# Kernel tuning notes

Hardware: AMD Instinct MI355X
Metric: run time of the kernel (lower is better)

The kernel has to match this reference:

```python
import jax, jax.numpy as jnp
import numpy as np

BITS = 4
GROUP_SIZE = 128
IN_FEATURES = 4096
OUT_FEATURES = 11008
PACKED_DIM = IN_FEATURES * BITS // 32  # 512
NUM_GROUPS = IN_FEATURES // GROUP_SIZE  # 32


def setup_inputs() -> dict:
    key = jax.random.key(0)
    k1, k2, k3, k4, k5 = jax.random.split(key, 5)
    x = jax.random.normal(k1, (4, 2048, IN_FEATURES), dtype=jnp.float32)
    # packed uint32 words stored as int32 bit pattern (full 32-bit entropy)
    weight_packed = jax.random.randint(
        k2, (OUT_FEATURES, PACKED_DIM), jnp.iinfo(jnp.int32).min, jnp.iinfo(jnp.int32).max, dtype=jnp.int32
    )
    scales = jax.random.uniform(k3, (OUT_FEATURES, NUM_GROUPS), dtype=jnp.float32, minval=0.01, maxval=0.1)
    biases = jax.random.normal(k4, (OUT_FEATURES, NUM_GROUPS), dtype=jnp.float32) * 0.1
    bias = jax.random.normal(k5, (OUT_FEATURES,), dtype=jnp.float32) * 0.1
    return {"x": x, "weight_packed": weight_packed, "scales": scales, "biases": biases, "bias": bias}


def _unpack_int4(weight_packed):
    # (O, packed_dim) int32 -> view as uint32, extract 8 nibbles per word -> (O, infeatures)
    w = weight_packed.astype(jnp.uint32)
    shifts = (jnp.arange(32 // BITS, dtype=jnp.uint32) * BITS)  # [0,4,...,28]
    mask = jnp.uint32((1 << BITS) - 1)
    nibbles = (w[:, :, None] >> shifts[None, None, :]) & mask  # (O, packed, 8)
    return nibbles.reshape(w.shape[0], -1)[:, :IN_FEATURES]


def _dequant_weight(weight_packed, scales, biases):
    intw = _unpack_int4(weight_packed).astype(jnp.float32)  # (O, I)
    s = jnp.repeat(scales, GROUP_SIZE, axis=1)[:, :IN_FEATURES]  # (O, I)
    b = jnp.repeat(biases, GROUP_SIZE, axis=1)[:, :IN_FEATURES]
    return s * intw + b


def reference(x, weight_packed, scales, biases, bias):
    W = _dequant_weight(weight_packed, scales, biases)  # (O, I)
    out = jnp.einsum("bsi,oi->bso", x, W)
    return out + bias
```

## Files before the change

### kernel.cpp

```cpp
#include <hip/hip_runtime.h>

#define K_DIM 4096
#define N_DIM 11008
#define M_DIM 8192
#define K2B (K_DIM * 2)

#define BM 128
#define BN 128
#define BK 32

typedef __bf16 bf16x8_t __attribute__((ext_vector_type(8)));
typedef float f32x4_t __attribute__((ext_vector_type(4)));

#define GLD_LDS16(g, l)                                                        \
  __builtin_amdgcn_global_load_lds(                                            \
      (const __attribute__((address_space(1))) void*)(g),                      \
      (__attribute__((address_space(3))) void*)(l), 16, 0, 0)

__global__ void dequant_w(const int* __restrict__ wp, const float* __restrict__ sc,
                          const float* __restrict__ bg, __bf16* __restrict__ W) {
  const int tid = blockIdx.x * 256 + threadIdx.x;
  const unsigned w = (unsigned)wp[tid];
  const int row = tid >> 9;
  const int word = tid & 511;
  const int g = word >> 4;
  const float s = sc[row * 32 + g];
  const float b = bg[row * 32 + g];
  bf16x8_t v;
#pragma unroll
  for (int i = 0; i < 8; ++i)
    v[i] = (__bf16)(s * (float)((w >> (4 * i)) & 15u) + b);
  ((bf16x8_t*)W)[tid] = v;
}

__global__ void cvt_x(const float* __restrict__ X, __bf16* __restrict__ Xb) {
  const size_t t = (size_t)blockIdx.x * 256 + threadIdx.x;
  const float4* s = ((const float4*)X) + 2 * t;
  const float4 f0 = s[0], f1 = s[1];
  bf16x8_t v;
  v[0] = (__bf16)f0.x; v[1] = (__bf16)f0.y; v[2] = (__bf16)f0.z; v[3] = (__bf16)f0.w;
  v[4] = (__bf16)f1.x; v[5] = (__bf16)f1.y; v[6] = (__bf16)f1.z; v[7] = (__bf16)f1.w;
  ((bf16x8_t*)Xb)[t] = v;
}

__device__ __forceinline__ void stage2(const char* g, char* l) {
  GLD_LDS16(g, l);
  GLD_LDS16(g + (size_t)64 * K2B, l + 8192);
}

template <int AM, int AN>
__device__ __forceinline__ void mfma_quad(f32x4_t (&acc)[8][4],
                                          const bf16x8_t (&A)[4][2],
                                          const bf16x8_t (&B)[2][2]) {
#pragma unroll
  for (int mi = 0; mi < 4; ++mi)
#pragma unroll
    for (int nj = 0; nj < 2; ++nj)
#pragma unroll
      for (int ks = 0; ks < 2; ++ks)
        acc[AM + mi][AN + nj] = __builtin_amdgcn_mfma_f32_16x16x32_bf16(
            A[mi][ks], B[nj][ks], acc[AM + mi][AN + nj], 0, 0, 0);
}

__device__ __forceinline__ void rd_a(bf16x8_t (&d)[4][2], const char* p, int s0, int s1) {
#pragma unroll
  for (int mi = 0; mi < 4; ++mi) {
    d[mi][0] = *(const bf16x8_t*)(p + mi * 2048 + s0);
    d[mi][1] = *(const bf16x8_t*)(p + mi * 2048 + s1);
  }
}
__device__ __forceinline__ void rd_b(bf16x8_t (&d)[2][2], const char* p, int s0, int s1) {
#pragma unroll
  for (int nj = 0; nj < 2; ++nj) {
    d[nj][0] = *(const bf16x8_t*)(p + nj * 2048 + s0);
    d[nj][1] = *(const bf16x8_t*)(p + nj * 2048 + s1);
  }
}

#define PH_SYNC_IN()                                                           \
  do {                                                                         \
    __builtin_amdgcn_s_barrier();                                              \
    asm volatile("s_waitcnt lgkmcnt(0)" ::: "memory");                         \
    __builtin_amdgcn_sched_barrier(0);                                         \
    __builtin_amdgcn_s_setprio(1);                                             \
  } while (0)
#define PH_SYNC_OUT()                                                          \
  do {                                                                         \
    __builtin_amdgcn_s_setprio(0);                                             \
    __builtin_amdgcn_sched_barrier(0);                                         \
    __builtin_amdgcn_s_barrier();                                              \
  } while (0)

__launch_bounds__(512, 2)
__global__ void qgemm8(const __bf16* __restrict__ Ab, const __bf16* __restrict__ Bw,
                       const float* __restrict__ bias, float* __restrict__ C) {
  __shared__ alignas(128) char smem[131072];
  const int tid = threadIdx.x;
  const int lane = tid & 63;
  const int wave = tid >> 6;
  const int wm = wave >> 2;
  const int wn = wave & 3;
  const int l16 = lane & 15;
  const int quad = lane >> 4;

  int bid = (int)blockIdx.x;
  bid = (bid & 7) * 172 + (bid >> 3);
  const int m0 = (bid / 43) * 256;
  const int n0 = (bid % 43) * 256;

  const int rr = tid >> 3;
  const int sw = ((tid & 7) ^ (rr & 7)) * 16;
  const char* gA = (const char*)Ab + (size_t)(m0 + rr) * K2B + sw;
  const char* gB = (const char*)Bw + (size_t)(n0 + rr) * K2B + sw;
  char* lA = smem + wave * 1024;
  char* lB = smem + 32768 + wave * 1024;

  const int s0 = ((0 + quad) ^ (l16 & 7)) * 16;
  const int s1 = ((4 + quad) ^ (l16 & 7)) * 16;
  const char* fA = smem + (wm * 64 + l16) * 128;
  const char* fB = smem + 32768 + (wn * 32 + l16) * 128;

  f32x4_t acc[8][4];
#pragma unroll
  for (int i = 0; i < 8; ++i)
#pragma unroll
    for (int j = 0; j < 4; ++j) acc[i][j] = (f32x4_t){0.f, 0.f, 0.f, 0.f};

  stage2(gA, lA);
  stage2(gA + (size_t)128 * K2B, lA + 16384);
  stage2(gB, lB);
  stage2(gB + (size_t)128 * K2B, lB + 16384);
  stage2(gA + 128, lA + 65536);
  stage2(gA + (size_t)128 * K2B + 128, lA + 65536 + 16384);
  stage2(gB + 128, lB + 65536);
  asm volatile("s_waitcnt vmcnt(6)" ::: "memory");
  __builtin_amdgcn_s_barrier();

  bf16x8_t fa0[4][2], fa1[4][2], fb0[2][2], fb1[2][2];

#pragma unroll 1
  for (int it = 0; it < 32; ++it) {
    const size_t o1 = (size_t)(2 * it + 1) * 128;
    const int tt2 = 2 * it + 2, tt3 = 2 * it + 3;
    const size_t o2 = (size_t)(tt2 < 64 ? tt2 : 63) * 128;
    const size_t o3 = (size_t)(tt3 < 64 ? tt3 : 63) * 128;

    rd_a(fa0, fA, s0, s1);
    rd_b(fb0, fB, s0, s1);
    stage2(gB + (size_t)128 * K2B + o1, lB + 65536 + 16384);
    PH_SYNC_IN();
    mfma_quad<0, 0>(acc, fa0, fb0);
    PH_SYNC_OUT();

    rd_a(fa1, fA + 16384, s0, s1);
    stage2(gA + o2, lA);
    PH_SYNC_IN();
    mfma_quad<4, 0>(acc, fa1, fb0);
    PH_SYNC_OUT();

    rd_b(fb1, fB + 16384, s0, s1);
    stage2(gA + (size_t)128 * K2B + o2, lA + 16384);
    PH_SYNC_IN();
    mfma_quad<4, 2>(acc, fa1, fb1);
    PH_SYNC_OUT();

    stage2(gB + o2, lB);
    asm volatile("s_waitcnt vmcnt(6)" ::: "memory");
    __builtin_amdgcn_s_barrier();
    __builtin_amdgcn_sched_barrier(0);
    __builtin_amdgcn_s_setprio(1);
    mfma_quad<0, 2>(acc, fa0, fb1);
    PH_SYNC_OUT();

    rd_a(fa0, fA + 65536, s0, s1);
    rd_b(fb0, fB + 65536, s0, s1);
    stage2(gB + (size_t)128 * K2B + o2, lB + 16384);
    PH_SYNC_IN();
    mfma_quad<0, 0>(acc, fa0, fb0);
    PH_SYNC_OUT();

    rd_a(fa1, fA + 65536 + 16384, s0, s1);
    stage2(gA + o3, lA + 65536);
    PH_SYNC_IN();
    mfma_quad<4, 0>(acc, fa1, fb0);
    PH_SYNC_OUT();

    rd_b(fb1, fB + 65536 + 16384, s0, s1);
    stage2(gA + (size_t)128 * K2B + o3, lA + 65536 + 16384);
    PH_SYNC_IN();
    mfma_quad<4, 2>(acc, fa1, fb1);
    PH_SYNC_OUT();

    stage2(gB + o3, lB + 65536);
    asm volatile("s_waitcnt vmcnt(6)" ::: "memory");
    __builtin_amdgcn_s_barrier();
    __builtin_amdgcn_sched_barrier(0);
    __builtin_amdgcn_s_setprio(1);
    mfma_quad<0, 2>(acc, fa0, fb1);
    PH_SYNC_OUT();
  }

  asm volatile("s_waitcnt vmcnt(0)" ::: "memory");

#pragma unroll
  for (int an = 0; an < 4; ++an) {
    const int n = n0 + (an >> 1) * 128 + wn * 32 + (an & 1) * 16 + l16;
    const float bv = bias[n];
#pragma unroll
    for (int am = 0; am < 8; ++am) {
      const int m = m0 + (am >> 2) * 128 + wm * 64 + (am & 3) * 16 + quad * 4;
#pragma unroll
      for (int r = 0; r < 4; ++r)
        C[(size_t)(m + r) * N_DIM + n] = acc[am][an][r] + bv;
    }
  }
}

template <int AMODE>
__launch_bounds__(256)
__global__ void qgemm(const __bf16* __restrict__ Ab, const float* __restrict__ Af,
                      const __bf16* __restrict__ Bw, const float* __restrict__ bias,
                      float* __restrict__ C) {
  __shared__ __bf16 As[BM * BK];
  __shared__ __bf16 Bs[BN * BK];

  const int tid = threadIdx.x;
  const int wave = tid >> 6;
  const int lane = tid & 63;
  const int l16 = lane & 15;
  const int quad = lane >> 4;
  const int wm = wave >> 1;
  const int wn = wave & 1;
  const int n0 = blockIdx.x * BN;
  const int m0 = blockIdx.y * BM;

  f32x4_t acc[4][4];
#pragma unroll
  for (int i = 0; i < 4; ++i)
#pragma unroll
    for (int j = 0; j < 4; ++j) acc[i][j] = (f32x4_t){0.f, 0.f, 0.f, 0.f};

  const int skq = lane & 3;
  const __bf16* gB0 =
      Bw + (size_t)(n0 + wave * 32 + (lane >> 2)) * K_DIM + skq * 8;
  __bf16* lB0 = Bs + (wave * 32) * BK;

  const __bf16* gA0 =
      (AMODE == 0) ? Ab + (size_t)(m0 + wave * 32 + (lane >> 2)) * K_DIM + skq * 8
                   : nullptr;
  __bf16* lA0 = As + (wave * 32) * BK;

  const int ar = tid >> 2;
  const int akq = tid & 3;
  const float* gX0 =
      (AMODE == 1) ? Af + (size_t)(m0 + ar) * K_DIM + akq * 8 : nullptr;
  __bf16* lAf = As + ar * BK + akq * 8;

  for (int kt = 0; kt < K_DIM; kt += BK) {
    __syncthreads();
    GLD_LDS16(gB0 + kt, lB0);
    GLD_LDS16(gB0 + kt + (size_t)16 * K_DIM, lB0 + 16 * BK);
    if (AMODE == 0) {
      GLD_LDS16(gA0 + kt, lA0);
      GLD_LDS16(gA0 + kt + (size_t)16 * K_DIM, lA0 + 16 * BK);
    } else {
#pragma unroll
      for (int p = 0; p < 2; ++p) {
        const float4* s = (const float4*)(gX0 + (size_t)p * 64 * K_DIM + kt);
        const float4 f0 = s[0], f1 = s[1];
        bf16x8_t v;
        v[0] = (__bf16)f0.x; v[1] = (__bf16)f0.y;
        v[2] = (__bf16)f0.z; v[3] = (__bf16)f0.w;
        v[4] = (__bf16)f1.x; v[5] = (__bf16)f1.y;
        v[6] = (__bf16)f1.z; v[7] = (__bf16)f1.w;
        *(bf16x8_t*)(lAf + p * 64 * BK) = v;
      }
    }
    __syncthreads();

    bf16x8_t fa[4], fb[4];
#pragma unroll
    for (int t = 0; t < 4; ++t)
      fa[t] = *(const bf16x8_t*)(As + (wm * 64 + t * 16 + l16) * BK + quad * 8);
#pragma unroll
    for (int t = 0; t < 4; ++t)
      fb[t] = *(const bf16x8_t*)(Bs + (wn * 64 + t * 16 + l16) * BK + quad * 8);
#pragma unroll
    for (int i = 0; i < 4; ++i)
#pragma unroll
      for (int j = 0; j < 4; ++j)
        acc[i][j] =
            __builtin_amdgcn_mfma_f32_16x16x32_bf16(fa[i], fb[j], acc[i][j], 0, 0, 0);
  }

#pragma unroll
  for (int j = 0; j < 4; ++j) {
    const int n = n0 + wn * 64 + j * 16 + l16;
    const float bv = bias[n];
#pragma unroll
    for (int i = 0; i < 4; ++i) {
      const int mb = m0 + wm * 64 + i * 16 + quad * 4;
#pragma unroll
      for (int r = 0; r < 4; ++r)
        C[(size_t)(mb + r) * N_DIM + n] = acc[i][j][r] + bv;
    }
  }
}

__global__ void qgemm_naive(const float* __restrict__ X, const int* __restrict__ WP,
                            const float* __restrict__ S, const float* __restrict__ BG,
                            const float* __restrict__ bias, float* __restrict__ C) {
  const int n = blockIdx.x * 256 + threadIdx.x;
  const int m = blockIdx.y;
  const float* x = X + (size_t)m * K_DIM;
  float acc = 0.f;
  for (int g = 0; g < 32; ++g) {
    const float s = S[n * 32 + g];
    const float b = BG[n * 32 + g];
    for (int wd = 0; wd < 16; ++wd) {
      const unsigned w = (unsigned)WP[n * 512 + g * 16 + wd];
      const int kb = g * 128 + wd * 8;
#pragma unroll
      for (int i = 0; i < 8; ++i)
        acc += (s * (float)((w >> (4 * i)) & 15u) + b) * x[kb + i];
    }
  }
  C[(size_t)m * N_DIM + n] = acc + bias[n];
}

extern "C" void kernel_launch(void* const* d_in, const int* in_sizes, int n_in,
                              void* d_out, int out_size, void* d_ws, size_t ws_size,
                              hipStream_t stream) {
  const float* X = (const float*)d_in[0];
  const int* WP = (const int*)d_in[1];
  const float* S = (const float*)d_in[2];
  const float* BG = (const float*)d_in[3];
  const float* BIAS = (const float*)d_in[4];
  float* C = (float*)d_out;

  const size_t needW = (size_t)N_DIM * K_DIM * 2;
  const size_t needX = (size_t)M_DIM * K_DIM * 2;

  if (ws_size >= needW + needX) {
    __bf16* W = (__bf16*)d_ws;
    __bf16* Xb = (__bf16*)((char*)d_ws + needW);
    dequant_w<<<(N_DIM * 512) / 256, 256, 0, stream>>>(WP, S, BG, W);
    cvt_x<<<(M_DIM * K_DIM) / (256 * 8), 256, 0, stream>>>(X, Xb);
    qgemm8<<<dim3((N_DIM / 256) * (M_DIM / 256)), 512, 0, stream>>>(Xb, W, BIAS, C);
  } else if (ws_size >= needW) {
    __bf16* W = (__bf16*)d_ws;
    dequant_w<<<(N_DIM * 512) / 256, 256, 0, stream>>>(WP, S, BG, W);
    qgemm<1><<<dim3(N_DIM / BN, M_DIM / BM), 256, 0, stream>>>(nullptr, X, W, BIAS, C);
  } else {
    qgemm_naive<<<dim3(N_DIM / 256, M_DIM), 256, 0, stream>>>(X, WP, S, BG, BIAS, C);
  }
}
```

Baseline: 1.065 ms.

## Split-K the tail GEMM tiles with atomic accumulation to balance the last wave

The 96 output tiles that would otherwise form a partial last wave are each split into two half-K blocks. The first 1280 tiles run at full K depth as before. A new init kernel first writes the bias into the tail region of C, and each half-K block then atomically adds its partial accumulators into that region. The aim is to cut wave-quantization idle time at the end of the GEMM. The cost is an extra kernel launch, float atomics on the tail tiles, and run-to-run nondeterministic summation order there.

```diff
diff --git a/kernel.cpp b/kernel.cpp
--- a/kernel.cpp
+++ b/kernel.cpp
@@ -41,6 +41,15 @@
   v[0] = (__bf16)f0.x; v[1] = (__bf16)f0.y; v[2] = (__bf16)f0.z; v[3] = (__bf16)f0.w;
   v[4] = (__bf16)f1.x; v[5] = (__bf16)f1.y; v[6] = (__bf16)f1.z; v[7] = (__bf16)f1.w;
   ((bf16x8_t*)Xb)[t] = v;
+}
+
+__global__ void init_ctail(const float* __restrict__ bias, float* __restrict__ C) {
+  const int t = 1280 + (blockIdx.x >> 8);
+  const int mi = blockIdx.x & 255;
+  const int m0 = (t / 43) * 256;
+  const int n0 = (t % 43) * 256;
+  const int n = n0 + threadIdx.x;
+  C[(size_t)(m0 + mi) * N_DIM + n] = bias[n];
 }
 
 __device__ __forceinline__ void stage2(const char* g, char* l) {
@@ -103,15 +112,28 @@
   const int l16 = lane & 15;
   const int quad = lane >> 4;
 
-  int bid = (int)blockIdx.x;
-  bid = (bid & 7) * 172 + (bid >> 3);
-  const int m0 = (bid / 43) * 256;
-  const int n0 = (bid % 43) * 256;
+  const int gid = (int)blockIdx.x;
+  const int x = gid & 7;
+  const int l = gid >> 3;
+  int tile, kh, nit;
+  if (l < 160) {
+    tile = x * 160 + l;
+    kh = 0;
+    nit = 32;
+  } else {
+    const int h = x * 24 + (l - 160);
+    tile = 1280 + (h >> 1);
+    kh = h & 1;
+    nit = 16;
+  }
+  const int m0 = (tile / 43) * 256;
+  const int n0 = (tile % 43) * 256;
+  const size_t kbase = (size_t)kh * 4096;
 
   const int rr = tid >> 3;
   const int sw = ((tid & 7) ^ (rr & 7)) * 16;
-  const char* gA = (const char*)Ab + (size_t)(m0 + rr) * K2B + sw;
-  const char* gB = (const char*)Bw + (size_t)(n0 + rr) * K2B + sw;
+  const char* gA = (const char*)Ab + (size_t)(m0 + rr) * K2B + sw + kbase;
+  const char* gB = (const char*)Bw + (size_t)(n0 + rr) * K2B + sw + kbase;
   char* lA = smem + wave * 1024;
   char* lB = smem + 32768 + wave * 1024;
 
@@ -137,13 +159,14 @@
   __builtin_amdgcn_s_barrier();
 
   bf16x8_t fa0[4][2], fa1[4][2], fb0[2][2], fb1[2][2];
+  const int kmaxt = 2 * nit - 1;
 
 #pragma unroll 1
-  for (int it = 0; it < 32; ++it) {
+  for (int it = 0; it < nit; ++it) {
     const size_t o1 = (size_t)(2 * it + 1) * 128;
     const int tt2 = 2 * it + 2, tt3 = 2 * it + 3;
-    const size_t o2 = (size_t)(tt2 < 64 ? tt2 : 63) * 128;
-    const size_t o3 = (size_t)(tt3 < 64 ? tt3 : 63) * 128;
+    const size_t o2 = (size_t)(tt2 < kmaxt ? tt2 : kmaxt) * 128;
+    const size_t o3 = (size_t)(tt3 < kmaxt ? tt3 : kmaxt) * 128;
 
     rd_a(fa0, fA, s0, s1);
     rd_b(fb0, fB, s0, s1);
@@ -202,16 +225,30 @@
 
   asm volatile("s_waitcnt vmcnt(0)" ::: "memory");
 
-#pragma unroll
-  for (int an = 0; an < 4; ++an) {
-    const int n = n0 + (an >> 1) * 128 + wn * 32 + (an & 1) * 16 + l16;
-    const float bv = bias[n];
-#pragma unroll
-    for (int am = 0; am < 8; ++am) {
-      const int m = m0 + (am >> 2) * 128 + wm * 64 + (am & 3) * 16 + quad * 4;
-#pragma unroll
-      for (int r = 0; r < 4; ++r)
-        C[(size_t)(m + r) * N_DIM + n] = acc[am][an][r] + bv;
+  if (nit == 32) {
+#pragma unroll
+    for (int an = 0; an < 4; ++an) {
+      const int n = n0 + (an >> 1) * 128 + wn * 32 + (an & 1) * 16 + l16;
+      const float bv = bias[n];
+#pragma unroll
+      for (int am = 0; am < 8; ++am) {
+        const int m = m0 + (am >> 2) * 128 + wm * 64 + (am & 3) * 16 + quad * 4;
+#pragma unroll
+        for (int r = 0; r < 4; ++r)
+          C[(size_t)(m + r) * N_DIM + n] = acc[am][an][r] + bv;
+      }
+    }
+  } else {
+#pragma unroll
+    for (int an = 0; an < 4; ++an) {
+      const int n = n0 + (an >> 1) * 128 + wn * 32 + (an & 1) * 16 + l16;
+#pragma unroll
+      for (int am = 0; am < 8; ++am) {
+        const int m = m0 + (am >> 2) * 128 + wm * 64 + (am & 3) * 16 + quad * 4;
+#pragma unroll
+        for (int r = 0; r < 4; ++r)
+          atomicAdd(&C[(size_t)(m + r) * N_DIM + n], acc[am][an][r]);
+      }
     }
   }
 }
@@ -346,7 +383,8 @@
     __bf16* Xb = (__bf16*)((char*)d_ws + needW);
     dequant_w<<<(N_DIM * 512) / 256, 256, 0, stream>>>(WP, S, BG, W);
     cvt_x<<<(M_DIM * K_DIM) / (256 * 8), 256, 0, stream>>>(X, Xb);
-    qgemm8<<<dim3((N_DIM / 256) * (M_DIM / 256)), 512, 0, stream>>>(Xb, W, BIAS, C);
+    init_ctail<<<96 * 256, 256, 0, stream>>>(BIAS, C);
+    qgemm8<<<dim3(1472), 512, 0, stream>>>(Xb, W, BIAS, C);
   } else if (ws_size >= needW) {
     __bf16* W = (__bf16*)d_ws;
     dequant_w<<<(N_DIM * 512) / 256, 256, 0, stream>>>(WP, S, BG, W);
```

After: 1.058 ms. About the same (-0.6%).
